# Kernel tuning notes

Measured on AMD Instinct MI355X. Metric: run time of the kernel, lower is better.

## Reference

```python
import jax, jax.numpy as jnp
import numpy as np

B, M, R = 1024, 2048, 8192  # batch of states, metabolites, reactions
SPARSITY = 0.002            # ~4 nonzero substrates / products per reaction


def setup_inputs() -> dict:
    key = jax.random.key(0)
    k1, k2, k3, k4, k5, k6 = jax.random.split(key, 6)
    # concentrations must be strictly positive (log used in power-law eval)
    conc = jax.random.uniform(k1, (B, M), minval=1e-3, maxval=1.0, dtype=jnp.float32)
    # sparse kinetic-order (exponent) matrix: ~4 substrates/reaction, order 1 or 2
    e_mask = jax.random.bernoulli(k2, SPARSITY, (M, R))
    E = jnp.where(e_mask, jax.random.randint(k3, (M, R), 1, 3), 0).astype(jnp.int32)
    # sparse stoichiometry matrix with coefficients in {-2,-1,1,2}
    s_mask = jax.random.bernoulli(k4, SPARSITY, (M, R))
    s_raw = jax.random.randint(k5, (M, R), 0, 4)
    s_val = jnp.where(s_raw < 2, s_raw - 2, s_raw - 1)  # {-2,-1,1,2}
    S = jnp.where(s_mask, s_val, 0).astype(jnp.int32)
    # per-reaction rate constants (the learned ParameterDict)
    k = jax.random.uniform(k6, (R,), minval=0.1, maxval=2.0, dtype=jnp.float32)
    return {"conc": conc, "E": E, "S": S, "k": k}


def reference(conc, E, S, k):
    # mass-action rate laws: v_j = k_j * prod_i c_i^{E_ij}, evaluated in log-space
    # logc: [B, M]; Ef: [M, R] -> v: [B, R]
    logc = jnp.log(conc)
    Ef = E.astype(conc.dtype)
    v = k * jnp.exp(jnp.einsum('bm,mr->br', logc, Ef))
    # stoichiometric ODE RHS: dX/dt = v @ S^T -> [B, M]
    Sf = S.astype(conc.dtype)
    dXdt = jnp.einsum('br,mr->bm', v, Sf)
    return dXdt
```

## Files before the change

kernel.cpp:

```cpp
#include <hip/hip_runtime.h>
#include <hip/hip_fp16.h>

#define Bsz 1024
#define Mm  2048
#define Rr  8192
#define EMAX 32
#define SMAX 64

typedef unsigned short ushort_t;

__global__ __launch_bounds__(256) void zero_ecnt(int* __restrict__ p) {
    p[blockIdx.x * 256 + threadIdx.x] = 0;
}

__global__ __launch_bounds__(256) void prep_kernel(
    const float* __restrict__ conc, const int* __restrict__ E, const int* __restrict__ S,
    __half2* __restrict__ logcTh2, int* __restrict__ ecnt, ushort_t* __restrict__ elist,
    int* __restrict__ scnt, ushort_t* __restrict__ slist)
{
    __shared__ float tile[64][65];
    __shared__ int n_hits;
    __shared__ int buf[256];
    const int bid = blockIdx.x;
    const int t   = threadIdx.x;

    if (bid < 512) {
        const int mt = (bid & 31) * 64;
        const int bt = (bid >> 5) * 64;
        const int lm = t & 63;
        const int w  = t >> 6;
        for (int i = w; i < 64; i += 4)
            tile[lm][i] = __logf(conc[(size_t)(bt + i) * Mm + mt + lm]);
        __syncthreads();
        const int s       = bt >> 7;
        const int colbase = (bt & 127) >> 1;
        __half2* dst = logcTh2 + (size_t)s * (Mm * 64);
        for (int idx = t; idx < 64 * 32; idx += 256) {
            const int j = idx >> 5, bp = idx & 31;
            dst[(mt + j) * 64 + colbase + bp] =
                __floats2half2_rn(tile[j][2 * bp], tile[j][2 * bp + 1]);
        }
    } else if (bid < 2560) {
        const int m = bid - 512;
        if (t == 0) n_hits = 0;
        __syncthreads();
        const int4* S4 = (const int4*)S + (size_t)m * 2048;
        int4 sv[8];
        #pragma unroll
        for (int u = 0; u < 8; ++u) sv[u] = S4[t + 256 * u];
        #pragma unroll
        for (int u = 0; u < 8; ++u) {
            const int r0 = (t + 256 * u) << 2;
            int v[4] = {sv[u].x, sv[u].y, sv[u].z, sv[u].w};
            #pragma unroll
            for (int q = 0; q < 4; ++q)
                if (v[q]) {
                    int i = atomicAdd(&n_hits, 1);
                    if (i < 256) buf[i] = ((v[q] + 2) << 13) | (r0 + q);
                }
        }
        __syncthreads();
        const int sn = min(n_hits, SMAX);
        if (t == 0) scnt[m] = sn;
        if (t < SMAX)
            slist[m * SMAX + t] = (t < sn) ? (ushort_t)buf[t]
                                           : (ushort_t)0x4000;
    } else {
        const int m = bid - 2560;
        if (t == 0) n_hits = 0;
        __syncthreads();
        const int4* E4 = (const int4*)E + (size_t)m * 2048;
        int4 ev[8];
        #pragma unroll
        for (int u = 0; u < 8; ++u) ev[u] = E4[t + 256 * u];
        #pragma unroll
        for (int u = 0; u < 8; ++u) {
            const int r0 = (t + 256 * u) << 2;
            int v[4] = {ev[u].x, ev[u].y, ev[u].z, ev[u].w};
            #pragma unroll
            for (int q = 0; q < 4; ++q)
                if (v[q]) {
                    int i = atomicAdd(&n_hits, 1);
                    if (i < 256) buf[i] = (v[q] << 13) | (r0 + q);
                }
        }
        __syncthreads();
        const int en = min(n_hits, 256);
        if (t < en) {
            int wv = buf[t];
            int r  = wv & 0x1FFF;
            int e  = wv >> 13;
            int slot = atomicAdd(&ecnt[r], 1);
            if (slot < EMAX) elist[r * EMAX + slot] = (ushort_t)((e << 11) | m);
        }
    }
}

__global__ __launch_bounds__(256) void rates_kernel(
    const __half2* __restrict__ logcTh2, const float* __restrict__ kvec,
    const int* __restrict__ ecnt, const ushort_t* __restrict__ elist,
    __half2* __restrict__ VTh)
{
    const int s   = blockIdx.x & 7;
    const int rch = blockIdx.x >> 3;
    const int col = threadIdx.x & 63;
    const int wr  = __builtin_amdgcn_readfirstlane(threadIdx.x >> 6);
    const __half2* lc = logcTh2 + (size_t)s * (Mm * 64);
    __half2* vt = VTh + (size_t)s * (Rr * 64);
    const int rb = rch * 32 + wr * 8;

    int  cnt[8]; int2 L0[8]; float kk[8];
    #pragma unroll
    for (int i = 0; i < 8; ++i) {
        const int r = rb + i;
        cnt[i] = ecnt[r];
        L0[i]  = *(const int2*)(elist + (r << 5));
        kk[i]  = kvec[r];
    }
    float2 acc[8];
    unsigned w; float2 g; float v0, v1;
    #define EG2(word, c0, c1, A)                                               \
        w = (unsigned)(word);                                                  \
        v0 = (c0) ? (float)((w & 0xFFFF) >> 11) : 0.f;                         \
        v1 = (c1) ? (float)(w >> 27) : 0.f;                                    \
        g = __half22float2(lc[(w & 0x7FF) * 64 + col]);                        \
        A.x += v0 * g.x;  A.y += v0 * g.y;                                     \
        g = __half22float2(lc[((w >> 16) & 0x7FF) * 64 + col]);                \
        A.x += v1 * g.x;  A.y += v1 * g.y;
    #pragma unroll
    for (int i = 0; i < 8; ++i) {
        acc[i] = make_float2(0.f, 0.f);
        EG2(L0[i].x, cnt[i] > 0, cnt[i] > 1, acc[i])
        EG2(L0[i].y, cnt[i] > 2, cnt[i] > 3, acc[i])
    }
    #pragma unroll
    for (int i = 0; i < 8; ++i) {
        for (int j = 4; j < cnt[i]; j += 4) {
            int2 T = *(const int2*)(elist + ((rb + i) << 5) + j);
            EG2(T.x, j + 0 < cnt[i], j + 1 < cnt[i], acc[i])
            EG2(T.y, j + 2 < cnt[i], j + 3 < cnt[i], acc[i])
        }
    }
    #undef EG2
    #pragma unroll
    for (int i = 0; i < 8; ++i)
        vt[(rb + i) * 64 + col] =
            __floats2half2_rn(kk[i] * __expf(acc[i].x), kk[i] * __expf(acc[i].y));
}

__global__ __launch_bounds__(256) void assemble_kernel(
    const __half2* __restrict__ VTh, const int* __restrict__ scnt,
    const ushort_t* __restrict__ slist, float* __restrict__ out)
{
    __shared__ float tile[128][17];
    const int s   = blockIdx.x & 7;
    const int mch = blockIdx.x >> 3;
    const int col = threadIdx.x & 63;
    const int wm  = __builtin_amdgcn_readfirstlane(threadIdx.x >> 6);
    const __half2* vt = VTh + (size_t)s * (Rr * 64);
    const int m0 = mch * 16;

    int scn[4]; int4 W0[4], W1[4];
    #pragma unroll
    for (int i = 0; i < 4; ++i) {
        const int m = m0 + i * 4 + wm;
        scn[i] = scnt[m];
        W0[i]  = *(const int4*)(slist + (m << 6));
        W1[i]  = *(const int4*)(slist + (m << 6) + 8);
    }
    unsigned w; float2 v; float sw;
    #define SG(word, A)                                                        \
        w = (unsigned)(word);                                                  \
        v = __half22float2(vt[(w & 0x1FFF) * 64 + col]);                       \
        sw = (float)((int)((w & 0xFFFF) >> 13) - 2);                           \
        A.x += sw * v.x;  A.y += sw * v.y;                                     \
        v = __half22float2(vt[((w >> 16) & 0x1FFF) * 64 + col]);               \
        sw = (float)((int)(w >> 29) - 2);                                      \
        A.x += sw * v.x;  A.y += sw * v.y;
    #pragma unroll
    for (int i = 0; i < 4; ++i) {
        const int ml = i * 4 + wm;
        float2 a = make_float2(0.f, 0.f);
        SG(W0[i].x, a) SG(W0[i].y, a) SG(W0[i].z, a) SG(W0[i].w, a)
        SG(W1[i].x, a) SG(W1[i].y, a) SG(W1[i].z, a) SG(W1[i].w, a)
        for (int j = 16; j < scn[i]; j += 8) {
            int4 T = *(const int4*)(slist + ((m0 + ml) << 6) + j);
            SG(T.x, a) SG(T.y, a) SG(T.z, a) SG(T.w, a)
        }
        tile[2 * col][ml]     = a.x;
        tile[2 * col + 1][ml] = a.y;
    }
    #undef SG
    __syncthreads();
    #pragma unroll
    for (int pass = 0; pass < 2; ++pass) {
        const int bl = (threadIdx.x >> 2) + pass * 64;
        const int fl = threadIdx.x & 3;
        float4 vv = *(const float4*)&tile[bl][fl * 4];
        *(float4*)(out + (size_t)(s * 128 + bl) * Mm + m0 + fl * 4) = vv;
    }
}

extern "C" void kernel_launch(void* const* d_in, const int* in_sizes, int n_in,
                              void* d_out, int out_size, void* d_ws, size_t ws_size,
                              hipStream_t stream) {
    const float* conc = (const float*)d_in[0];
    const int*   E    = (const int*)d_in[1];
    const int*   S    = (const int*)d_in[2];
    const float* kvec = (const float*)d_in[3];
    float* out = (float*)d_out;

    __half2* VTh     = (__half2*)d_ws;
    __half2* logcTh2 = (__half2*)((char*)d_ws + (size_t)Rr * Bsz * sizeof(__half));
    int*    ecnt     = (int*)((char*)logcTh2 + (size_t)Mm * Bsz * sizeof(__half));
    int*    scnt     = ecnt + Rr;
    ushort_t* elist  = (ushort_t*)(scnt + Mm);
    ushort_t* slist  = elist + Rr * EMAX;
    const size_t need = (size_t)Rr * Bsz * sizeof(__half)
                      + (size_t)Mm * Bsz * sizeof(__half)
                      + (size_t)(Rr + Mm) * sizeof(int)
                      + (size_t)(Rr * EMAX + Mm * SMAX) * sizeof(ushort_t);
    if (ws_size < need) return;

    zero_ecnt<<<32, 256, 0, stream>>>(ecnt);
    prep_kernel<<<4608, 256, 0, stream>>>(conc, E, S, logcTh2, ecnt, elist, scnt, slist);
    rates_kernel<<<2048, 256, 0, stream>>>(logcTh2, kvec, ecnt, elist, VTh);
    assemble_kernel<<<1024, 256, 0, stream>>>(VTh, scnt, slist, out);
}
```

Before: 181.6 us.

## Move S-list construction into rates kernel to overlap with rate evaluation

Building the stoichiometry lists moves out of the prep kernel and into a merged kernel whose blocks interleave S-scan work with rate evaluation. The streaming read of the S matrix, which is memory bound, can then run alongside the gather-heavy rate computation instead of lengthening the prep kernel. The prep kernel now handles only logc transposition and E-list building, and its shared memory is unified into one buffer. Counts are clamped to EMAX/SMAX on read, and the merged kernel grows from 2048 to 4096 blocks, half of which are S-scan blocks.

```diff
diff --git a/kernel.cpp b/kernel.cpp
--- a/kernel.cpp
+++ b/kernel.cpp
@@ -14,17 +14,15 @@
 }
 
 __global__ __launch_bounds__(256) void prep_kernel(
-    const float* __restrict__ conc, const int* __restrict__ E, const int* __restrict__ S,
-    __half2* __restrict__ logcTh2, int* __restrict__ ecnt, ushort_t* __restrict__ elist,
-    int* __restrict__ scnt, ushort_t* __restrict__ slist)
+    const float* __restrict__ conc, const int* __restrict__ E,
+    __half2* __restrict__ logcTh2, int* __restrict__ ecnt, ushort_t* __restrict__ elist)
 {
-    __shared__ float tile[64][65];
-    __shared__ int n_hits;
-    __shared__ int buf[256];
+    __shared__ int smem[64 * 65 + 1];
     const int bid = blockIdx.x;
     const int t   = threadIdx.x;
 
     if (bid < 512) {
+        float (*tile)[65] = (float(*)[65])smem;
         const int mt = (bid & 31) * 64;
         const int bt = (bid >> 5) * 64;
         const int lm = t & 63;
@@ -40,9 +38,56 @@
             dst[(mt + j) * 64 + colbase + bp] =
                 __floats2half2_rn(tile[j][2 * bp], tile[j][2 * bp + 1]);
         }
-    } else if (bid < 2560) {
+    } else {
         const int m = bid - 512;
-        if (t == 0) n_hits = 0;
+        int* buf = smem;
+        int* nh  = smem + 256;
+        if (t == 0) *nh = 0;
+        __syncthreads();
+        const int4* E4 = (const int4*)E + (size_t)m * 2048;
+        int4 ev[8];
+        #pragma unroll
+        for (int u = 0; u < 8; ++u) ev[u] = E4[t + 256 * u];
+        #pragma unroll
+        for (int u = 0; u < 8; ++u) {
+            const int r0 = (t + 256 * u) << 2;
+            int v[4] = {ev[u].x, ev[u].y, ev[u].z, ev[u].w};
+            #pragma unroll
+            for (int q = 0; q < 4; ++q)
+                if (v[q]) {
+                    int i = atomicAdd(nh, 1);
+                    if (i < 256) buf[i] = (v[q] << 13) | (r0 + q);
+                }
+        }
+        __syncthreads();
+        const int en = min(*nh, 256);
+        if (t < en) {
+            int wv = buf[t];
+            int r  = wv & 0x1FFF;
+            int e  = wv >> 13;
+            int slot = atomicAdd(&ecnt[r], 1);
+            if (slot < EMAX) elist[r * EMAX + slot] = (ushort_t)((e << 11) | m);
+        }
+    }
+}
+
+__global__ __launch_bounds__(256) void rs_kernel(
+    const __half2* __restrict__ logcTh2, const float* __restrict__ kvec,
+    const int* __restrict__ ecnt, const ushort_t* __restrict__ elist,
+    const int* __restrict__ S, int* __restrict__ scnt, ushort_t* __restrict__ slist,
+    __half2* __restrict__ VTh)
+{
+    __shared__ int smem[257];
+    const int bid   = blockIdx.x;
+    const int t     = threadIdx.x;
+    const int grp   = bid >> 3;
+    const int lane8 = bid & 7;
+
+    if ((grp & 1) == 0) {
+        const int m = (grp >> 1) * 8 + lane8;
+        int* buf = smem;
+        int* nh  = smem + 256;
+        if (t == 0) *nh = 0;
         __syncthreads();
         const int4* S4 = (const int4*)S + (size_t)m * 2048;
         int4 sv[8];
@@ -55,56 +100,22 @@
             #pragma unroll
             for (int q = 0; q < 4; ++q)
                 if (v[q]) {
-                    int i = atomicAdd(&n_hits, 1);
+                    int i = atomicAdd(nh, 1);
                     if (i < 256) buf[i] = ((v[q] + 2) << 13) | (r0 + q);
                 }
         }
         __syncthreads();
-        const int sn = min(n_hits, SMAX);
+        const int sn = min(*nh, SMAX);
         if (t == 0) scnt[m] = sn;
         if (t < SMAX)
             slist[m * SMAX + t] = (t < sn) ? (ushort_t)buf[t]
                                            : (ushort_t)0x4000;
-    } else {
-        const int m = bid - 2560;
-        if (t == 0) n_hits = 0;
-        __syncthreads();
-        const int4* E4 = (const int4*)E + (size_t)m * 2048;
-        int4 ev[8];
-        #pragma unroll
-        for (int u = 0; u < 8; ++u) ev[u] = E4[t + 256 * u];
-        #pragma unroll
-        for (int u = 0; u < 8; ++u) {
-            const int r0 = (t + 256 * u) << 2;
-            int v[4] = {ev[u].x, ev[u].y, ev[u].z, ev[u].w};
-            #pragma unroll
-            for (int q = 0; q < 4; ++q)
-                if (v[q]) {
-                    int i = atomicAdd(&n_hits, 1);
-                    if (i < 256) buf[i] = (v[q] << 13) | (r0 + q);
-                }
-        }
-        __syncthreads();
-        const int en = min(n_hits, 256);
-        if (t < en) {
-            int wv = buf[t];
-            int r  = wv & 0x1FFF;
-            int e  = wv >> 13;
-            int slot = atomicAdd(&ecnt[r], 1);
-            if (slot < EMAX) elist[r * EMAX + slot] = (ushort_t)((e << 11) | m);
-        }
-    }
-}
-
-__global__ __launch_bounds__(256) void rates_kernel(
-    const __half2* __restrict__ logcTh2, const float* __restrict__ kvec,
-    const int* __restrict__ ecnt, const ushort_t* __restrict__ elist,
-    __half2* __restrict__ VTh)
-{
-    const int s   = blockIdx.x & 7;
-    const int rch = blockIdx.x >> 3;
-    const int col = threadIdx.x & 63;
-    const int wr  = __builtin_amdgcn_readfirstlane(threadIdx.x >> 6);
+        return;
+    }
+    const int s   = lane8;
+    const int rch = grp >> 1;
+    const int col = t & 63;
+    const int wr  = __builtin_amdgcn_readfirstlane(t >> 6);
     const __half2* lc = logcTh2 + (size_t)s * (Mm * 64);
     __half2* vt = VTh + (size_t)s * (Rr * 64);
     const int rb = rch * 32 + wr * 8;
@@ -113,7 +124,7 @@
     #pragma unroll
     for (int i = 0; i < 8; ++i) {
         const int r = rb + i;
-        cnt[i] = ecnt[r];
+        cnt[i] = min(ecnt[r], EMAX);
         L0[i]  = *(const int2*)(elist + (r << 5));
         kk[i]  = kvec[r];
     }
@@ -164,7 +175,7 @@
     #pragma unroll
     for (int i = 0; i < 4; ++i) {
         const int m = m0 + i * 4 + wm;
-        scn[i] = scnt[m];
+        scn[i] = min(scnt[m], SMAX);
         W0[i]  = *(const int4*)(slist + (m << 6));
         W1[i]  = *(const int4*)(slist + (m << 6) + 8);
     }
@@ -223,7 +234,7 @@
     if (ws_size < need) return;
 
     zero_ecnt<<<32, 256, 0, stream>>>(ecnt);
-    prep_kernel<<<4608, 256, 0, stream>>>(conc, E, S, logcTh2, ecnt, elist, scnt, slist);
-    rates_kernel<<<2048, 256, 0, stream>>>(logcTh2, kvec, ecnt, elist, VTh);
+    prep_kernel<<<2560, 256, 0, stream>>>(conc, E, logcTh2, ecnt, elist);
+    rs_kernel<<<4096, 256, 0, stream>>>(logcTh2, kvec, ecnt, elist, S, scnt, slist, VTh);
     assemble_kernel<<<1024, 256, 0, stream>>>(VTh, scnt, slist, out);
 }
```

Result: faster. 174.6 us (median of 2 runs) (-3.9%).

## Fuse rate evaluation into stoichiometric assembly and drop the intermediate rate buffer

Applied to the files above, without the earlier changes.

The separate rates and assemble kernels are merged into one kernel. For each metabolite, it walks the reactions in that metabolite's stoichiometry list and recomputes each reaction's rate inline by gathering log-concentrations and applying exp. This removes the fp16 rate buffer of reactions by batch, its global write and gather-read traffic, and one kernel launch. In exchange, each rate is recomputed once for every metabolite it touches, which multiplies the log-concentration gathers and exp work. The per-block metabolite tile is also halved to 8 rows.

```diff
diff --git a/kernel.cpp b/kernel.cpp
--- a/kernel.cpp
+++ b/kernel.cpp
@@ -96,109 +96,83 @@
     }
 }
 
-__global__ __launch_bounds__(256) void rates_kernel(
+#define EG2(word, c0, c1, A)                                                   \
+    w = (unsigned)(word);                                                      \
+    v0 = (c0) ? (float)((w & 0xFFFF) >> 11) : 0.f;                             \
+    v1 = (c1) ? (float)(w >> 27) : 0.f;                                        \
+    g = __half22float2(lc[(w & 0x7FF) * 64 + col]);                            \
+    A.x += v0 * g.x;  A.y += v0 * g.y;                                         \
+    g = __half22float2(lc[((w >> 16) & 0x7FF) * 64 + col]);                    \
+    A.x += v1 * g.x;  A.y += v1 * g.y;
+
+__device__ __forceinline__ void acc8(
+    const int4 W, const __half2* __restrict__ lc, const float* __restrict__ kvec,
+    const int* __restrict__ ecnt, const ushort_t* __restrict__ elist,
+    const int col, float2& a)
+{
+    unsigned pw[4] = {(unsigned)W.x, (unsigned)W.y, (unsigned)W.z, (unsigned)W.w};
+    int rr[8]; float sww[8]; int cc[8]; int2 LL[8]; float kk[8];
+    #pragma unroll
+    for (int q = 0; q < 8; ++q) {
+        const unsigned w16 = (pw[q >> 1] >> ((q & 1) * 16)) & 0xFFFFu;
+        rr[q]  = (int)(w16 & 0x1FFF);
+        sww[q] = (float)((int)(w16 >> 13) - 2);
+    }
+    #pragma unroll
+    for (int q = 0; q < 8; ++q) {
+        cc[q] = min(ecnt[rr[q]], EMAX);
+        LL[q] = *(const int2*)(elist + (rr[q] << 5));
+        kk[q] = kvec[rr[q]];
+    }
+    unsigned w; float2 g; float v0, v1;
+    #pragma unroll
+    for (int q = 0; q < 8; ++q) {
+        float2 acc2 = make_float2(0.f, 0.f);
+        EG2(LL[q].x, cc[q] > 0, cc[q] > 1, acc2)
+        EG2(LL[q].y, cc[q] > 2, cc[q] > 3, acc2)
+        for (int j = 4; j < cc[q]; j += 4) {
+            int2 T = *(const int2*)(elist + (rr[q] << 5) + j);
+            EG2(T.x, j + 0 < cc[q], j + 1 < cc[q], acc2)
+            EG2(T.y, j + 2 < cc[q], j + 3 < cc[q], acc2)
+        }
+        a.x += sww[q] * kk[q] * __expf(acc2.x);
+        a.y += sww[q] * kk[q] * __expf(acc2.y);
+    }
+}
+
+__global__ __launch_bounds__(256) void ra_kernel(
     const __half2* __restrict__ logcTh2, const float* __restrict__ kvec,
     const int* __restrict__ ecnt, const ushort_t* __restrict__ elist,
-    __half2* __restrict__ VTh)
+    const int* __restrict__ scnt, const ushort_t* __restrict__ slist,
+    float* __restrict__ out)
 {
-    const int s   = blockIdx.x & 7;
-    const int rch = blockIdx.x >> 3;
-    const int col = threadIdx.x & 63;
-    const int wr  = __builtin_amdgcn_readfirstlane(threadIdx.x >> 6);
-    const __half2* lc = logcTh2 + (size_t)s * (Mm * 64);
-    __half2* vt = VTh + (size_t)s * (Rr * 64);
-    const int rb = rch * 32 + wr * 8;
-
-    int  cnt[8]; int2 L0[8]; float kk[8];
-    #pragma unroll
-    for (int i = 0; i < 8; ++i) {
-        const int r = rb + i;
-        cnt[i] = ecnt[r];
-        L0[i]  = *(const int2*)(elist + (r << 5));
-        kk[i]  = kvec[r];
-    }
-    float2 acc[8];
-    unsigned w; float2 g; float v0, v1;
-    #define EG2(word, c0, c1, A)                                               \
-        w = (unsigned)(word);                                                  \
-        v0 = (c0) ? (float)((w & 0xFFFF) >> 11) : 0.f;                         \
-        v1 = (c1) ? (float)(w >> 27) : 0.f;                                    \
-        g = __half22float2(lc[(w & 0x7FF) * 64 + col]);                        \
-        A.x += v0 * g.x;  A.y += v0 * g.y;                                     \
-        g = __half22float2(lc[((w >> 16) & 0x7FF) * 64 + col]);                \
-        A.x += v1 * g.x;  A.y += v1 * g.y;
-    #pragma unroll
-    for (int i = 0; i < 8; ++i) {
-        acc[i] = make_float2(0.f, 0.f);
-        EG2(L0[i].x, cnt[i] > 0, cnt[i] > 1, acc[i])
-        EG2(L0[i].y, cnt[i] > 2, cnt[i] > 3, acc[i])
-    }
-    #pragma unroll
-    for (int i = 0; i < 8; ++i) {
-        for (int j = 4; j < cnt[i]; j += 4) {
-            int2 T = *(const int2*)(elist + ((rb + i) << 5) + j);
-            EG2(T.x, j + 0 < cnt[i], j + 1 < cnt[i], acc[i])
-            EG2(T.y, j + 2 < cnt[i], j + 3 < cnt[i], acc[i])
-        }
-    }
-    #undef EG2
-    #pragma unroll
-    for (int i = 0; i < 8; ++i)
-        vt[(rb + i) * 64 + col] =
-            __floats2half2_rn(kk[i] * __expf(acc[i].x), kk[i] * __expf(acc[i].y));
-}
-
-__global__ __launch_bounds__(256) void assemble_kernel(
-    const __half2* __restrict__ VTh, const int* __restrict__ scnt,
-    const ushort_t* __restrict__ slist, float* __restrict__ out)
-{
-    __shared__ float tile[128][17];
+    __shared__ float tile[128][9];
     const int s   = blockIdx.x & 7;
     const int mch = blockIdx.x >> 3;
     const int col = threadIdx.x & 63;
     const int wm  = __builtin_amdgcn_readfirstlane(threadIdx.x >> 6);
-    const __half2* vt = VTh + (size_t)s * (Rr * 64);
-    const int m0 = mch * 16;
-
-    int scn[4]; int4 W0[4], W1[4];
-    #pragma unroll
-    for (int i = 0; i < 4; ++i) {
-        const int m = m0 + i * 4 + wm;
-        scn[i] = scnt[m];
-        W0[i]  = *(const int4*)(slist + (m << 6));
-        W1[i]  = *(const int4*)(slist + (m << 6) + 8);
-    }
-    unsigned w; float2 v; float sw;
-    #define SG(word, A)                                                        \
-        w = (unsigned)(word);                                                  \
-        v = __half22float2(vt[(w & 0x1FFF) * 64 + col]);                       \
-        sw = (float)((int)((w & 0xFFFF) >> 13) - 2);                           \
-        A.x += sw * v.x;  A.y += sw * v.y;                                     \
-        v = __half22float2(vt[((w >> 16) & 0x1FFF) * 64 + col]);               \
-        sw = (float)((int)(w >> 29) - 2);                                      \
-        A.x += sw * v.x;  A.y += sw * v.y;
-    #pragma unroll
-    for (int i = 0; i < 4; ++i) {
+    const __half2* lc = logcTh2 + (size_t)s * (Mm * 64);
+    const int m0 = mch * 8;
+
+    #pragma unroll
+    for (int i = 0; i < 2; ++i) {
+        const int m  = m0 + i * 4 + wm;
+        const int sn = min(scnt[m], SMAX);
+        const int4* SL = (const int4*)(slist + (m << 6));
+        float2 a = make_float2(0.f, 0.f);
+        acc8(SL[0], lc, kvec, ecnt, elist, col, a);
+        acc8(SL[1], lc, kvec, ecnt, elist, col, a);
+        for (int j = 16; j < sn; j += 8)
+            acc8(SL[j >> 3], lc, kvec, ecnt, elist, col, a);
         const int ml = i * 4 + wm;
-        float2 a = make_float2(0.f, 0.f);
-        SG(W0[i].x, a) SG(W0[i].y, a) SG(W0[i].z, a) SG(W0[i].w, a)
-        SG(W1[i].x, a) SG(W1[i].y, a) SG(W1[i].z, a) SG(W1[i].w, a)
-        for (int j = 16; j < scn[i]; j += 8) {
-            int4 T = *(const int4*)(slist + ((m0 + ml) << 6) + j);
-            SG(T.x, a) SG(T.y, a) SG(T.z, a) SG(T.w, a)
-        }
         tile[2 * col][ml]     = a.x;
         tile[2 * col + 1][ml] = a.y;
     }
-    #undef SG
     __syncthreads();
-    #pragma unroll
-    for (int pass = 0; pass < 2; ++pass) {
-        const int bl = (threadIdx.x >> 2) + pass * 64;
-        const int fl = threadIdx.x & 3;
-        float4 vv = *(const float4*)&tile[bl][fl * 4];
-        *(float4*)(out + (size_t)(s * 128 + bl) * Mm + m0 + fl * 4) = vv;
-    }
+    const int bl = threadIdx.x >> 1;
+    const int fl = threadIdx.x & 1;
+    float4 vv = *(const float4*)&tile[bl][fl * 4];
+    *(float4*)(out + (size_t)(s * 128 + bl) * Mm + m0 + fl * 4) = vv;
 }
 
 extern "C" void kernel_launch(void* const* d_in, const int* in_sizes, int n_in,
@@ -210,20 +184,17 @@
     const float* kvec = (const float*)d_in[3];
     float* out = (float*)d_out;
 
-    __half2* VTh     = (__half2*)d_ws;
-    __half2* logcTh2 = (__half2*)((char*)d_ws + (size_t)Rr * Bsz * sizeof(__half));
+    __half2* logcTh2 = (__half2*)d_ws;
     int*    ecnt     = (int*)((char*)logcTh2 + (size_t)Mm * Bsz * sizeof(__half));
     int*    scnt     = ecnt + Rr;
     ushort_t* elist  = (ushort_t*)(scnt + Mm);
     ushort_t* slist  = elist + Rr * EMAX;
-    const size_t need = (size_t)Rr * Bsz * sizeof(__half)
-                      + (size_t)Mm * Bsz * sizeof(__half)
+    const size_t need = (size_t)Mm * Bsz * sizeof(__half)
                       + (size_t)(Rr + Mm) * sizeof(int)
                       + (size_t)(Rr * EMAX + Mm * SMAX) * sizeof(ushort_t);
     if (ws_size < need) return;
 
     zero_ecnt<<<32, 256, 0, stream>>>(ecnt);
     prep_kernel<<<4608, 256, 0, stream>>>(conc, E, S, logcTh2, ecnt, elist, scnt, slist);
-    rates_kernel<<<2048, 256, 0, stream>>>(logcTh2, kvec, ecnt, elist, VTh);
-    assemble_kernel<<<1024, 256, 0, stream>>>(VTh, scnt, slist, out);
-}
+    ra_kernel<<<2048, 256, 0, stream>>>(logcTh2, kvec, ecnt, elist, scnt, slist, out);
+}
```

Result: slower. 210.6 us (+16.0%).
